# Kernel optimization log

Measured on AMD Instinct MI355X. Metric: run time of the kernel, lower is better.

Reference implementation:

```python
import jax, jax.numpy as jnp
import numpy as np

N = 10000      # nodes
ND = 64        # node_dim
H = 128        # hidden_dim
L = 4          # num_layers
K = 16         # knn k
TD = 16        # time_dim


def _time_embed(t, n):
    # sinusoidal embedding, matches _time_embed: freqs = exp(linspace(0,1,half)*-4)
    half = TD // 2
    freqs = jnp.exp(jnp.linspace(0.0, 1.0, half) * -4.0)            # [half]
    angles = t.reshape(1, 1) * freqs[None, :]                        # [1, half]
    emb = jnp.concatenate([jnp.sin(angles), jnp.cos(angles)], -1)    # [1, TD]
    return jnp.broadcast_to(emb, (n, TD))


def _knn_edges(pos, k):
    # full cdist + topk, mirroring _knn_graph (no_grad in torch)
    n = pos.shape[0]
    sq = jnp.sum(pos * pos, -1)
    d2 = sq[:, None] + sq[None, :] - 2.0 * (pos @ pos.T)             # [N, N]
    idxr = jnp.arange(n)
    d2 = d2.at[idxr, idxr].set(jnp.inf)
    _, nbr = jax.lax.top_k(-d2, k)                                   # [N, K] nearest
    src = jnp.repeat(idxr, k)
    dst = nbr.reshape(-1)
    return src, dst


def _egnn_layer(h, pos, src, dst, s, ew1, eb1, ew2, eb2, nw1, nb1, nw2, nb2, cw, cb):
    n = h.shape[0]
    diff = pos[dst] - pos[src]                                       # [E, 3]
    r2 = jnp.sum(diff * diff, -1, keepdims=True)                     # [E, 1]
    r = jnp.sqrt(r2 + 1e-8)
    dir_ij = diff / r
    e_in = jnp.concatenate([h[dst], h[src], r2], -1)                 # [E, 2H+1]
    m = jax.nn.silu(e_in @ ew1 + eb1)
    m = jax.nn.silu(m @ ew2 + eb2)                                   # [E, H]
    m = m * s[src][:, None]                                          # s-gate
    m_sum = jax.ops.segment_sum(m, dst, num_segments=n)              # [N, H]
    deg = jax.ops.segment_sum(jnp.ones((m.shape[0], 1), m.dtype), dst, num_segments=n)
    deg = jnp.maximum(deg, 1.0)
    m_sum = m_sum / deg
    hn = jax.nn.silu(jnp.concatenate([h, m_sum], -1) @ nw1 + nb1)
    h_new = hn @ nw2 + nb2                                           # [N, H]
    gamma = m @ cw + cb                                              # [E, 1]
    cu = jax.ops.segment_sum(gamma * dir_ij, dst, num_segments=n) / deg
    return h_new, pos + cu


def setup_inputs() -> dict:
    key = jax.random.key(0)
    ks = jax.random.split(key, 24)
    g = lambda k, shape: (jax.random.normal(k, shape, dtype=jnp.float32) * 0.05)
    z = lambda shape: jnp.zeros(shape, jnp.float32)
    return {
        'x': jax.random.normal(ks[0], (N, ND), jnp.float32),
        'pos': jax.random.normal(ks[1], (N, 3), jnp.float32) * 5.0,
        't': jax.random.uniform(ks[2], (1,), jnp.float32),
        's': jax.random.uniform(ks[3], (N,), jnp.float32),
        'proj_w': g(ks[4], (ND + 1 + TD, H)), 'proj_b': z((H,)),
        'edge_w1': g(ks[5], (L, 2 * H + 1, H)), 'edge_b1': z((L, H)),
        'edge_w2': g(ks[6], (L, H, H)), 'edge_b2': z((L, H)),
        'node_w1': g(ks[7], (L, 2 * H, H)), 'node_b1': z((L, H)),
        'node_w2': g(ks[8], (L, H, H)), 'node_b2': z((L, H)),
        'coord_w': g(ks[9], (L, H, 1)), 'coord_b': z((L, 1)),
        'ec_w': g(ks[10], (H, 3)), 'ec_b': z((3,)),
        'ef_w': g(ks[11], (H, ND)), 'ef_b': z((ND,)),
    }


def reference(x, pos, t, s, proj_w, proj_b, edge_w1, edge_b1, edge_w2, edge_b2,
              node_w1, node_b1, node_w2, node_b2, coord_w, coord_b,
              ec_w, ec_b, ef_w, ef_b):
    n = x.shape[0]
    src, dst = _knn_edges(jax.lax.stop_gradient(pos), K)  # graph build is no_grad
    temb = _time_embed(t[0], n)
    h = jnp.concatenate([x, s[:, None], temb], -1) @ proj_w + proj_b  # [N, H]
    p = pos
    for l in range(L):
        h, p = _egnn_layer(h, p, src, dst, s,
                           edge_w1[l], edge_b1[l], edge_w2[l], edge_b2[l],
                           node_w1[l], node_b1[l], node_w2[l], node_b2[l],
                           coord_w[l], coord_b[l])
    eps_c = h @ ec_w + ec_b                                           # [N, 3]
    eps_f = h @ ef_w + ef_b                                           # [N, ND]
    return jnp.concatenate([eps_c, eps_f, p], -1)                     # [N, 3+ND+3]
```

## Files before the change

kernel.cpp:

```cpp
#include <hip/hip_runtime.h>
#include <math.h>

#define N_NODES 10000
#define ND 64
#define H 128
#define LAYERS 4
#define KNN 16
#define TD 16
#define E_EDGES (N_NODES * KNN)
#define KC 1250
#define TILE_E 128

typedef __attribute__((ext_vector_type(8))) short short8;
typedef __attribute__((ext_vector_type(4))) float f32x4;

__device__ __forceinline__ float silu(float x) {
  return x * __builtin_amdgcn_rcpf(1.0f + __expf(-x));
}

__device__ __forceinline__ unsigned short f2bf(float f) {
  unsigned int u = __float_as_uint(f);
  u += 0x7fffu + ((u >> 16) & 1u);
  return (unsigned short)(u >> 16);
}
__device__ __forceinline__ float bf2f(unsigned short h) {
  return __uint_as_float(((unsigned int)h) << 16);
}

__global__ __launch_bounds__(256) void pos4_kernel(const float* __restrict__ pos,
                                                   float4* __restrict__ pos4,
                                                   float* __restrict__ p0,
                                                   int* __restrict__ degi) {
  int i = blockIdx.x * 256 + threadIdx.x;
  if (i >= N_NODES) return;
  float x = pos[i * 3 + 0], y = pos[i * 3 + 1], z = pos[i * 3 + 2];
  pos4[i] = make_float4(x, y, z, x * x + y * y + z * z);
  p0[i * 3 + 0] = x;
  p0[i * 3 + 1] = y;
  p0[i * 3 + 2] = z;
  degi[i] = 0;
}

__global__ __launch_bounds__(256) void wcvt_kernel(
    const float* __restrict__ ew2, const float* __restrict__ nw1,
    const float* __restrict__ nw2, const float* __restrict__ ew1,
    const float* __restrict__ pw, const float* __restrict__ ecw,
    const float* __restrict__ efw, unsigned short* __restrict__ w2T,
    unsigned short* __restrict__ nw1T, unsigned short* __restrict__ nw2T,
    unsigned short* __restrict__ ew1T, unsigned short* __restrict__ pwT,
    unsigned short* __restrict__ owT) {
  int i = blockIdx.x * 256 + threadIdx.x;
  if (i < 65536) {
    int l = i >> 14, rem = i & 16383, c = rem >> 7, o = rem & 127;
    w2T[l * 16384 + o * 128 + c] = f2bf(ew2[i]);
  } else if (i < 196608) {
    int j = i - 65536;
    int l = j >> 15, rem = j & 32767, c2 = rem >> 7, o = rem & 127;
    nw1T[l * 32768 + o * 256 + c2] = f2bf(nw1[j]);
  } else if (i < 262144) {
    int j = i - 196608;
    int l = j >> 14, rem = j & 16383, c = rem >> 7, o = rem & 127;
    nw2T[l * 16384 + o * 128 + c] = f2bf(nw2[j]);
  } else if (i < 393216) {
    int j = i - 262144;
    int l = j >> 15, rem = j & 32767, r = rem >> 7, o = rem & 127;
    int o2 = o + ((r >> 7) << 7);
    int c = r & 127;
    ew1T[l * 32768 + o2 * 128 + c] = f2bf(ew1[l * 257 * 128 + r * 128 + o]);
  } else if (i < 405504) {
    int j = i - 393216;
    int o = j / 96, c = j - o * 96;
    pwT[j] = (c < 81) ? f2bf(pw[c * 128 + o]) : 0;
  } else {
    int j = i - 405504;
    int o = j >> 7, c = j & 127;
    float v = 0.0f;
    if (o < 3) v = ecw[c * 3 + o];
    else if (o < 67) v = efw[c * 64 + (o - 3)];
    owT[j] = f2bf(v);
  }
}

#define INS(dval, gbase, V, ID, TH)                                   \
  {                                                                   \
    unsigned long long mask = __ballot((dval) < (TH));                \
    while (mask) {                                                    \
      int sl = __ffsll((long long)mask) - 1;                          \
      mask &= mask - 1;                                               \
      float db = __shfl((dval), sl, 64);                              \
      if (db >= (TH)) continue;                                       \
      int gj = (gbase) + sl;                                          \
      float pv = __shfl_up((V), 1, 64);                               \
      int pid = __shfl_up((ID), 1, 64);                               \
      bool stay = ((V) <= db);                                        \
      bool tk = (lane == 0) || (pv <= db);                            \
      (V) = stay ? (V) : (tk ? db : pv);                              \
      (ID) = stay ? (ID) : (tk ? gj : pid);                           \
      (TH) = __shfl((V), 16, 64);                                     \
    }                                                                 \
  }

__global__ __launch_bounds__(256) void knn_kernel(const float4* __restrict__ pos4,
                                                  int* __restrict__ nbr,
                                                  int* __restrict__ degi) {
  __shared__ float4 C[KC];
  int tid = threadIdx.x;
  int lane = tid & 63;
  int wid = tid >> 6;
  int qb = blockIdx.x * 8 + wid * 2;
  float4 q0 = pos4[qb];
  float4 q1 = pos4[qb + 1];
  float v0 = __builtin_inff(), v1 = __builtin_inff();
  int id0 = 0, id1 = 0;
  float th0 = __builtin_inff(), th1 = __builtin_inff();
  for (int base = 0; base < N_NODES; base += KC) {
    int cnt = min(KC, N_NODES - base);
    __syncthreads();
    for (int jj = tid; jj < cnt; jj += 256) C[jj] = pos4[base + jj];
    __syncthreads();
    for (int j0 = 0; j0 < cnt; j0 += 256) {
      float dA0 = __builtin_inff(), dA1 = __builtin_inff();
      float dB0 = __builtin_inff(), dB1 = __builtin_inff();
      float dC0 = __builtin_inff(), dC1 = __builtin_inff();
      float dD0 = __builtin_inff(), dD1 = __builtin_inff();
      int ja = j0 + lane, jbx = j0 + 64 + lane;
      int jc = j0 + 128 + lane, jd = j0 + 192 + lane;
      if (ja < cnt) {
        float4 p = C[ja];
        dA0 = fmaf(-2.0f, fmaf(q0.x, p.x, fmaf(q0.y, p.y, q0.z * p.z)), p.w);
        dA1 = fmaf(-2.0f, fmaf(q1.x, p.x, fmaf(q1.y, p.y, q1.z * p.z)), p.w);
      }
      if (jbx < cnt) {
        float4 p = C[jbx];
        dB0 = fmaf(-2.0f, fmaf(q0.x, p.x, fmaf(q0.y, p.y, q0.z * p.z)), p.w);
        dB1 = fmaf(-2.0f, fmaf(q1.x, p.x, fmaf(q1.y, p.y, q1.z * p.z)), p.w);
      }
      if (jc < cnt) {
        float4 p = C[jc];
        dC0 = fmaf(-2.0f, fmaf(q0.x, p.x, fmaf(q0.y, p.y, q0.z * p.z)), p.w);
        dC1 = fmaf(-2.0f, fmaf(q1.x, p.x, fmaf(q1.y, p.y, q1.z * p.z)), p.w);
      }
      if (jd < cnt) {
        float4 p = C[jd];
        dD0 = fmaf(-2.0f, fmaf(q0.x, p.x, fmaf(q0.y, p.y, q0.z * p.z)), p.w);
        dD1 = fmaf(-2.0f, fmaf(q1.x, p.x, fmaf(q1.y, p.y, q1.z * p.z)), p.w);
      }
      int gb = base + j0;
      float m0 = fminf(fminf(dA0, dB0), fminf(dC0, dD0));
      if (__ballot(m0 < th0)) {
        INS(dA0, gb, v0, id0, th0);
        INS(dB0, gb + 64, v0, id0, th0);
        INS(dC0, gb + 128, v0, id0, th0);
        INS(dD0, gb + 192, v0, id0, th0);
      }
      float m1 = fminf(fminf(dA1, dB1), fminf(dC1, dD1));
      if (__ballot(m1 < th1)) {
        INS(dA1, gb, v1, id1, th1);
        INS(dB1, gb + 64, v1, id1, th1);
        INS(dC1, gb + 128, v1, id1, th1);
        INS(dD1, gb + 192, v1, id1, th1);
      }
    }
  }
  if (lane >= 1 && lane < 17) {
    nbr[qb * KNN + lane - 1] = id0;
    atomicAdd(&degi[id0], 1);
    nbr[(qb + 1) * KNN + lane - 1] = id1;
    atomicAdd(&degi[id1], 1);
  }
}

__global__ __launch_bounds__(1024) void scan_kernel(const int* __restrict__ degi,
                                                    int* __restrict__ off,
                                                    int* __restrict__ cursor) {
  __shared__ int part[1024];
  int t = threadIdx.x;
  int base = t * 10;
  int sum = 0;
  if (t < 1000)
    for (int i = 0; i < 10; ++i) sum += degi[base + i];
  part[t] = sum;
  __syncthreads();
  for (int stp = 1; stp < 1024; stp <<= 1) {
    int v = (t >= stp) ? part[t - stp] : 0;
    __syncthreads();
    part[t] += v;
    __syncthreads();
  }
  if (t < 1000) {
    int run = (t == 0) ? 0 : part[t - 1];
    for (int i = 0; i < 10; ++i) {
      off[base + i] = run;
      cursor[base + i] = run;
      run += degi[base + i];
    }
  }
  if (t == 0) off[N_NODES] = E_EDGES;
}

__global__ void scatter_kernel(const int* __restrict__ nbr, int* __restrict__ cursor,
                               int* __restrict__ eid, int* __restrict__ dstof) {
  int e = blockIdx.x * 256 + threadIdx.x;
  if (e < E_EDGES) {
    int d = nbr[e];
    int p = atomicAdd(&cursor[d], 1);
    eid[p] = e;
    dstof[p] = d;
  }
}

__global__ void sort_kernel(const int* __restrict__ off, int* __restrict__ eid) {
  int n = blockIdx.x * 256 + threadIdx.x;
  if (n >= N_NODES) return;
  int a = off[n], b = off[n + 1];
  for (int i = a + 1; i < b; ++i) {
    int v = eid[i];
    int j = i - 1;
    while (j >= a && eid[j] > v) { eid[j + 1] = eid[j]; --j; }
    eid[j + 1] = v;
  }
}

__global__ __launch_bounds__(256) void proj_ab_kernel(
    const float* __restrict__ x, const float* __restrict__ s,
    const float* __restrict__ tptr, const unsigned short* __restrict__ pwT,
    const float* __restrict__ pb, const unsigned short* __restrict__ ew1T,
    const float* __restrict__ eb1, float* __restrict__ h_out,
    unsigned short* __restrict__ Abf, unsigned short* __restrict__ Bbf) {
  __shared__ unsigned short inpb[16][104];
  __shared__ unsigned short hb[16][136];
  int tid = threadIdx.x;
  int n0 = blockIdx.x * 16;
  float t = tptr[0];
  for (int idx = tid; idx < 16 * 104; idx += 256) {
    int n = idx / 104, c = idx - n * 104;
    int gn = n0 + n;
    float val;
    if (c < 64) val = x[gn * ND + c];
    else if (c == 64) val = s[gn];
    else if (c < 81) {
      int j = c - 65;
      int jj = (j < 8) ? j : (j - 8);
      float f = __expf(-4.0f * (float)jj / 7.0f);
      float a = t * f;
      val = (j < 8) ? sinf(a) : cosf(a);
    } else val = 0.0f;
    inpb[n][c] = f2bf(val);
  }
  __syncthreads();
  int w = tid >> 6, lane = tid & 63, fr = lane & 15, kg = lane >> 4;
  f32x4 acc[2];
  acc[0] = (f32x4){0.f, 0.f, 0.f, 0.f};
  acc[1] = (f32x4){0.f, 0.f, 0.f, 0.f};
#pragma unroll
  for (int ks = 0; ks < 3; ++ks) {
    int k = ks * 32 + kg * 8;
    short8 a = *(const short8*)&inpb[fr][k];
#pragma unroll
    for (int nt = 0; nt < 2; ++nt) {
      int col = w * 32 + nt * 16 + fr;
      short8 b = *(const short8*)&pwT[col * 96 + k];
      acc[nt] = __builtin_amdgcn_mfma_f32_16x16x32_bf16(a, b, acc[nt], 0, 0, 0);
    }
  }
#pragma unroll
  for (int nt = 0; nt < 2; ++nt) {
    int col = w * 32 + nt * 16 + fr;
    float bias = pb[col];
#pragma unroll
    for (int r = 0; r < 4; ++r) {
      int row = kg * 4 + r;
      float hv = acc[nt][r] + bias;
      h_out[(n0 + row) * H + col] = hv;
      hb[row][col] = f2bf(hv);
    }
  }
  __syncthreads();
  f32x4 acc2[4];
#pragma unroll
  for (int nt = 0; nt < 4; ++nt) acc2[nt] = (f32x4){0.f, 0.f, 0.f, 0.f};
#pragma unroll
  for (int ks = 0; ks < 4; ++ks) {
    int k = ks * 32 + kg * 8;
    short8 a = *(const short8*)&hb[fr][k];
#pragma unroll
    for (int nt = 0; nt < 4; ++nt) {
      int col = w * 64 + nt * 16 + fr;
      short8 b = *(const short8*)&ew1T[col * H + k];
      acc2[nt] = __builtin_amdgcn_mfma_f32_16x16x32_bf16(a, b, acc2[nt], 0, 0, 0);
    }
  }
#pragma unroll
  for (int nt = 0; nt < 4; ++nt) {
    int col = w * 64 + nt * 16 + fr;
    float bias = (col < H) ? eb1[col] : 0.0f;
#pragma unroll
    for (int r = 0; r < 4; ++r) {
      int row = kg * 4 + r;
      float val = acc2[nt][r] + bias;
      if (col < H) Abf[(n0 + row) * H + col] = f2bf(val);
      else Bbf[(n0 + row) * H + (col - H)] = f2bf(val);
    }
  }
}

__global__ __launch_bounds__(256) void edge_mfma_kernel(
    const unsigned short* __restrict__ Abf, const unsigned short* __restrict__ Bbf,
    const float* __restrict__ p, const float* __restrict__ s,
    const int* __restrict__ csr_off, const int* __restrict__ eid,
    const int* __restrict__ dstof, const float* __restrict__ wr,
    const unsigned short* __restrict__ w2T, const float* __restrict__ eb2,
    const float* __restrict__ cw, const float* __restrict__ cbp,
    float* __restrict__ msA, float* __restrict__ msB,
    float* __restrict__ cuA, float* __restrict__ cuB) {
  __shared__ unsigned short t1s[TILE_E][136];
  __shared__ float r2A[TILE_E], sA[TILE_E], dirA[TILE_E][3], gA[TILE_E];
  __shared__ float gpart[2][TILE_E];
  __shared__ int srcA[TILE_E], dstA[TILE_E];
  __shared__ float wrs[H], b2s[H], cws[H];

  int tid = threadIdx.x;
  int P0 = blockIdx.x * TILE_E;
  int P1 = P0 + TILE_E;

  if (tid < H) { wrs[tid] = wr[tid]; b2s[tid] = eb2[tid]; cws[tid] = cw[tid]; }
  if (tid < TILE_E) {
    int e = tid;
    int edge = eid[P0 + e];
    int src = edge >> 4;
    int d = dstof[P0 + e];
    srcA[e] = src;
    dstA[e] = d;
    float dx = p[d * 3 + 0] - p[src * 3 + 0];
    float dy = p[d * 3 + 1] - p[src * 3 + 1];
    float dz = p[d * 3 + 2] - p[src * 3 + 2];
    float r2 = dx * dx + dy * dy + dz * dz;
    r2A[e] = r2;
    float rinv = 1.0f / sqrtf(r2 + 1e-8f);
    dirA[e][0] = dx * rinv;
    dirA[e][1] = dy * rinv;
    dirA[e][2] = dz * rinv;
    sA[e] = s[src];
  }
  __syncthreads();

  int nA = dstA[0], nB = dstA[TILE_E - 1];
  int nn = nB - nA + 1;

  for (int idx = tid; idx < TILE_E * 32; idx += 256) {
    int e = idx >> 5, cp = (idx & 31) * 4;
    uint2 au = *(const uint2*)&Abf[dstA[e] * H + cp];
    uint2 bu = *(const uint2*)&Bbf[srcA[e] * H + cp];
    float r2v = r2A[e];
    float pr0 = silu(bf2f((unsigned short)(au.x & 0xffffu)) +
                     bf2f((unsigned short)(bu.x & 0xffffu)) + r2v * wrs[cp]);
    float pr1 = silu(bf2f((unsigned short)(au.x >> 16)) +
                     bf2f((unsigned short)(bu.x >> 16)) + r2v * wrs[cp + 1]);
    float pr2 = silu(bf2f((unsigned short)(au.y & 0xffffu)) +
                     bf2f((unsigned short)(bu.y & 0xffffu)) + r2v * wrs[cp + 2]);
    float pr3 = silu(bf2f((unsigned short)(au.y >> 16)) +
                     bf2f((unsigned short)(bu.y >> 16)) + r2v * wrs[cp + 3]);
    uint2 o;
    o.x = ((unsigned int)f2bf(pr1) << 16) | (unsigned int)f2bf(pr0);
    o.y = ((unsigned int)f2bf(pr3) << 16) | (unsigned int)f2bf(pr2);
    *(uint2*)&t1s[e][cp] = o;
  }
  __syncthreads();

  int w = tid >> 6, lane = tid & 63;
  int fr = lane & 15, kg = lane >> 4;
  f32x4 acc[8][2];
#pragma unroll
  for (int mt = 0; mt < 8; ++mt)
#pragma unroll
    for (int nt = 0; nt < 2; ++nt) acc[mt][nt] = (f32x4){0.f, 0.f, 0.f, 0.f};
#pragma unroll
  for (int ks = 0; ks < 4; ++ks) {
    int k = ks * 32 + kg * 8;
    short8 bf0 = *(const short8*)&w2T[(w * 32 + fr) * H + k];
    short8 bf1 = *(const short8*)&w2T[(w * 32 + 16 + fr) * H + k];
#pragma unroll
    for (int mt = 0; mt < 8; ++mt) {
      short8 a = *(const short8*)&t1s[mt * 16 + fr][k];
      acc[mt][0] = __builtin_amdgcn_mfma_f32_16x16x32_bf16(a, bf0, acc[mt][0], 0, 0, 0);
      acc[mt][1] = __builtin_amdgcn_mfma_f32_16x16x32_bf16(a, bf1, acc[mt][1], 0, 0, 0);
    }
  }
  __syncthreads();

#pragma unroll
  for (int mt = 0; mt < 8; ++mt) {
#pragma unroll
    for (int nt = 0; nt < 2; ++nt) {
      int col = w * 32 + nt * 16 + fr;
      float b2v = b2s[col];
#pragma unroll
      for (int r = 0; r < 4; ++r) {
        int row = mt * 16 + kg * 4 + r;
        float mv = silu(acc[mt][nt][r] + b2v) * sA[row];
        t1s[row][col] = f2bf(mv);
      }
    }
  }
  __syncthreads();

  {
    int e = tid & 127, half = tid >> 7;
    int c0 = half * 64;
    float g = 0.f;
    for (int c = c0; c < c0 + 64; c += 4) {
      uint2 u = *(const uint2*)&t1s[e][c];
      g = fmaf(bf2f((unsigned short)(u.x & 0xffffu)), cws[c], g);
      g = fmaf(bf2f((unsigned short)(u.x >> 16)), cws[c + 1], g);
      g = fmaf(bf2f((unsigned short)(u.y & 0xffffu)), cws[c + 2], g);
      g = fmaf(bf2f((unsigned short)(u.y >> 16)), cws[c + 3], g);
    }
    gpart[half][e] = g;
  }
  __syncthreads();
  if (tid < TILE_E) gA[tid] = gpart[0][tid] + gpart[1][tid] + cbp[0];
  __syncthreads();

  for (int idx = tid; idx < nn * 32; idx += 256) {
    int ni = idx >> 5, cq = (idx & 31) * 4;
    int n = nA + ni;
    int o0 = csr_off[n], o1 = csr_off[n + 1];
    int lo = max(o0, P0), hi = min(o1, P1);
    float s0 = 0.f, s1 = 0.f, s2 = 0.f, s3 = 0.f;
    for (int pos = lo; pos < hi; ++pos) {
      uint2 u = *(const uint2*)&t1s[pos - P0][cq];
      s0 += bf2f((unsigned short)(u.x & 0xffffu));
      s1 += bf2f((unsigned short)(u.x >> 16));
      s2 += bf2f((unsigned short)(u.y & 0xffffu));
      s3 += bf2f((unsigned short)(u.y >> 16));
    }
    float4 sv = make_float4(s0, s1, s2, s3);
    if (o0 >= P0) {
      *(float4*)&msA[n * H + cq] = sv;
      if (o1 <= P1) *(float4*)&msB[n * H + cq] = make_float4(0.f, 0.f, 0.f, 0.f);
    } else {
      *(float4*)&msB[n * H + cq] = sv;
    }
  }
  for (int idx = tid; idx < nn * 3; idx += 256) {
    int ni = idx / 3, comp = idx - ni * 3;
    int n = nA + ni;
    int o0 = csr_off[n], o1 = csr_off[n + 1];
    int lo = max(o0, P0), hi = min(o1, P1);
    float sum = 0.f;
    for (int pos = lo; pos < hi; ++pos)
      sum += gA[pos - P0] * dirA[pos - P0][comp];
    if (o0 >= P0) {
      cuA[n * 3 + comp] = sum;
      if (o1 <= P1) cuB[n * 3 + comp] = 0.0f;
    } else {
      cuB[n * 3 + comp] = sum;
    }
  }
}

__global__ __launch_bounds__(256) void node_mfma_kernel(
    const float* __restrict__ h, const float* __restrict__ msA,
    const float* __restrict__ msB, const int* __restrict__ degi,
    const float* __restrict__ cuA, const float* __restrict__ cuB,
    const float* __restrict__ p_in, const unsigned short* __restrict__ w1T,
    const float* __restrict__ nb1, const unsigned short* __restrict__ w2T,
    const float* __restrict__ nb2, const unsigned short* __restrict__ ew1Tn,
    const float* __restrict__ eb1n, int doab, float* __restrict__ h_out,
    float* __restrict__ p_out, unsigned short* __restrict__ Abf,
    unsigned short* __restrict__ Bbf) {
  __shared__ unsigned short insb[16][264];
  __shared__ unsigned short hnsb[16][136];
  int tid = threadIdx.x;
  int n0 = blockIdx.x * 16;
  for (int idx = tid; idx < 16 * H; idx += 256) {
    int n = idx >> 7, c = idx & 127;
    int gn = n0 + n;
    float hv = h[gn * H + c];
    int dg = degi[gn];
    float ms = 0.f;
    if (dg > 0) ms = (msA[gn * H + c] + msB[gn * H + c]) / (float)dg;
    insb[n][c] = f2bf(hv);
    insb[n][H + c] = f2bf(ms);
  }
  __syncthreads();
  int w = tid >> 6, lane = tid & 63, fr = lane & 15, kg = lane >> 4;
  f32x4 acc[2];
  acc[0] = (f32x4){0.f, 0.f, 0.f, 0.f};
  acc[1] = (f32x4){0.f, 0.f, 0.f, 0.f};
#pragma unroll
  for (int ks = 0; ks < 8; ++ks) {
    int k = ks * 32 + kg * 8;
    short8 a = *(const short8*)&insb[fr][k];
#pragma unroll
    for (int nt = 0; nt < 2; ++nt) {
      int col = w * 32 + nt * 16 + fr;
      short8 b = *(const short8*)&w1T[col * 256 + k];
      acc[nt] = __builtin_amdgcn_mfma_f32_16x16x32_bf16(a, b, acc[nt], 0, 0, 0);
    }
  }
#pragma unroll
  for (int nt = 0; nt < 2; ++nt) {
    int col = w * 32 + nt * 16 + fr;
    float b1 = nb1[col];
#pragma unroll
    for (int r = 0; r < 4; ++r) {
      int row = kg * 4 + r;
      hnsb[row][col] = f2bf(silu(acc[nt][r] + b1));
    }
  }
  __syncthreads();
  f32x4 acc2[2];
  acc2[0] = (f32x4){0.f, 0.f, 0.f, 0.f};
  acc2[1] = (f32x4){0.f, 0.f, 0.f, 0.f};
#pragma unroll
  for (int ks = 0; ks < 4; ++ks) {
    int k = ks * 32 + kg * 8;
    short8 a = *(const short8*)&hnsb[fr][k];
#pragma unroll
    for (int nt = 0; nt < 2; ++nt) {
      int col = w * 32 + nt * 16 + fr;
      short8 b = *(const short8*)&w2T[col * H + k];
      acc2[nt] = __builtin_amdgcn_mfma_f32_16x16x32_bf16(a, b, acc2[nt], 0, 0, 0);
    }
  }
  unsigned short (*hb)[136] = (unsigned short(*)[136])insb;
#pragma unroll
  for (int nt = 0; nt < 2; ++nt) {
    int col = w * 32 + nt * 16 + fr;
    float b2 = nb2[col];
#pragma unroll
    for (int r = 0; r < 4; ++r) {
      int row = kg * 4 + r;
      float hv = acc2[nt][r] + b2;
      h_out[(n0 + row) * H + col] = hv;
      hb[row][col] = f2bf(hv);
    }
  }
  if (tid < 48) {
    int nl = tid / 3, comp = tid - nl * 3;
    int gn = n0 + nl;
    int dg = degi[gn];
    float add = 0.0f;
    if (dg > 0)
      add = (cuA[gn * 3 + comp] + cuB[gn * 3 + comp]) / (float)dg;
    p_out[gn * 3 + comp] = p_in[gn * 3 + comp] + add;
  }
  if (doab) {
    __syncthreads();
    f32x4 acc3[4];
#pragma unroll
    for (int nt = 0; nt < 4; ++nt) acc3[nt] = (f32x4){0.f, 0.f, 0.f, 0.f};
#pragma unroll
    for (int ks = 0; ks < 4; ++ks) {
      int k = ks * 32 + kg * 8;
      short8 a = *(const short8*)&hb[fr][k];
#pragma unroll
      for (int nt = 0; nt < 4; ++nt) {
        int col = w * 64 + nt * 16 + fr;
        short8 b = *(const short8*)&ew1Tn[col * H + k];
        acc3[nt] = __builtin_amdgcn_mfma_f32_16x16x32_bf16(a, b, acc3[nt], 0, 0, 0);
      }
    }
#pragma unroll
    for (int nt = 0; nt < 4; ++nt) {
      int col = w * 64 + nt * 16 + fr;
      float bias = (col < H) ? eb1n[col] : 0.0f;
#pragma unroll
      for (int r = 0; r < 4; ++r) {
        int row = kg * 4 + r;
        float val = acc3[nt][r] + bias;
        if (col < H) Abf[(n0 + row) * H + col] = f2bf(val);
        else Bbf[(n0 + row) * H + (col - H)] = f2bf(val);
      }
    }
  }
}

__global__ __launch_bounds__(256) void out_mfma_kernel(
    const float* __restrict__ h, const float* __restrict__ p,
    const unsigned short* __restrict__ owT, const float* __restrict__ ecb,
    const float* __restrict__ efb, float* __restrict__ out) {
  __shared__ unsigned short hb[16][136];
  int tid = threadIdx.x;
  int n0 = blockIdx.x * 16;
  for (int idx = tid; idx < 16 * H; idx += 256) {
    int n = idx >> 7, c = idx & 127;
    hb[n][c] = f2bf(h[(n0 + n) * H + c]);
  }
  __syncthreads();
  int w = tid >> 6, lane = tid & 63, fr = lane & 15, kg = lane >> 4;
  int ntiles = (w == 0) ? 2 : 1;
  for (int tt = 0; tt < ntiles; ++tt) {
    int tile = (tt == 0) ? w : 4;
    f32x4 acc = (f32x4){0.f, 0.f, 0.f, 0.f};
    int col = tile * 16 + fr;
#pragma unroll
    for (int ks = 0; ks < 4; ++ks) {
      int k = ks * 32 + kg * 8;
      short8 a = *(const short8*)&hb[fr][k];
      short8 b = *(const short8*)&owT[col * H + k];
      acc = __builtin_amdgcn_mfma_f32_16x16x32_bf16(a, b, acc, 0, 0, 0);
    }
    if (col < 67) {
      float bias = (col < 3) ? ecb[col] : efb[col - 3];
#pragma unroll
      for (int r = 0; r < 4; ++r) {
        int row = kg * 4 + r;
        out[(n0 + row) * 70 + col] = acc[r] + bias;
      }
    }
  }
  if (tid < 48) {
    int nl = tid / 3, comp = tid - nl * 3;
    int gn = n0 + nl;
    out[gn * 70 + 67 + comp] = p[gn * 3 + comp];
  }
}

extern "C" void kernel_launch(void* const* d_in, const int* in_sizes, int n_in,
                              void* d_out, int out_size, void* d_ws, size_t ws_size,
                              hipStream_t stream) {
  const float* x = (const float*)d_in[0];
  const float* pos = (const float*)d_in[1];
  const float* t = (const float*)d_in[2];
  const float* s = (const float*)d_in[3];
  const float* pw = (const float*)d_in[4];
  const float* pb = (const float*)d_in[5];
  const float* ew1 = (const float*)d_in[6];
  const float* eb1 = (const float*)d_in[7];
  const float* ew2 = (const float*)d_in[8];
  const float* eb2 = (const float*)d_in[9];
  const float* nw1 = (const float*)d_in[10];
  const float* nb1 = (const float*)d_in[11];
  const float* nw2 = (const float*)d_in[12];
  const float* nb2 = (const float*)d_in[13];
  const float* cw = (const float*)d_in[14];
  const float* cb = (const float*)d_in[15];
  const float* ecw = (const float*)d_in[16];
  const float* ecb = (const float*)d_in[17];
  const float* efw = (const float*)d_in[18];
  const float* efb = (const float*)d_in[19];

  char* wp = (char*)d_ws;
  auto alloc = [&](size_t bytes) {
    char* r = wp;
    wp += (bytes + 255) & ~(size_t)255;
    return r;
  };
  float* h0 = (float*)alloc((size_t)N_NODES * H * 4);
  float* h1 = (float*)alloc((size_t)N_NODES * H * 4);
  unsigned short* Abf = (unsigned short*)alloc((size_t)N_NODES * H * 2);
  unsigned short* Bbf = (unsigned short*)alloc((size_t)N_NODES * H * 2);
  float* msAb = (float*)alloc((size_t)N_NODES * H * 4);
  float* msBb = (float*)alloc((size_t)N_NODES * H * 4);
  float* cuAb = (float*)alloc((size_t)N_NODES * 3 * 4);
  float* cuBb = (float*)alloc((size_t)N_NODES * 3 * 4);
  float* p0 = (float*)alloc((size_t)N_NODES * 3 * 4);
  float* p1 = (float*)alloc((size_t)N_NODES * 3 * 4);
  int* degi = (int*)alloc((size_t)N_NODES * 4);
  int* nbr = (int*)alloc((size_t)E_EDGES * 4);
  int* off = (int*)alloc((size_t)(N_NODES + 1) * 4);
  int* cursor = (int*)alloc((size_t)N_NODES * 4);
  int* eid = (int*)alloc((size_t)E_EDGES * 4);
  int* dstof = (int*)alloc((size_t)E_EDGES * 4);
  unsigned short* w2Tb = (unsigned short*)alloc((size_t)LAYERS * H * H * 2);
  unsigned short* nw1Tb = (unsigned short*)alloc((size_t)LAYERS * 2 * H * H * 2);
  unsigned short* nw2Tb = (unsigned short*)alloc((size_t)LAYERS * H * H * 2);
  unsigned short* ew1Tb = (unsigned short*)alloc((size_t)LAYERS * 2 * H * H * 2);
  unsigned short* pwTb = (unsigned short*)alloc((size_t)H * 96 * 2);
  unsigned short* owTb = (unsigned short*)alloc((size_t)80 * H * 2);

  float4* pos4 = (float4*)msAb;

  wcvt_kernel<<<1624, 256, 0, stream>>>(ew2, nw1, nw2, ew1, pw, ecw, efw,
                                        w2Tb, nw1Tb, nw2Tb, ew1Tb, pwTb, owTb);
  pos4_kernel<<<(N_NODES + 255) / 256, 256, 0, stream>>>(pos, pos4, p0, degi);
  knn_kernel<<<N_NODES / 8, 256, 0, stream>>>(pos4, nbr, degi);
  scan_kernel<<<1, 1024, 0, stream>>>(degi, off, cursor);
  scatter_kernel<<<(E_EDGES + 255) / 256, 256, 0, stream>>>(nbr, cursor, eid, dstof);
  sort_kernel<<<(N_NODES + 255) / 256, 256, 0, stream>>>(off, eid);
  proj_ab_kernel<<<N_NODES / 16, 256, 0, stream>>>(x, s, t, pwTb, pb, ew1Tb, eb1,
                                                   h0, Abf, Bbf);

  float* hc = h0;
  float* hn = h1;
  float* pc = p0;
  float* pn = p1;
  for (int l = 0; l < LAYERS; ++l) {
    const float* ew1l = ew1 + (size_t)l * 257 * H;
    int doab = (l < LAYERS - 1) ? 1 : 0;
    edge_mfma_kernel<<<E_EDGES / TILE_E, 256, 0, stream>>>(
        Abf, Bbf, pc, s, off, eid, dstof, ew1l + 256 * H,
        w2Tb + (size_t)l * H * H, eb2 + l * H, cw + l * H, cb + l,
        msAb, msBb, cuAb, cuBb);
    node_mfma_kernel<<<N_NODES / 16, 256, 0, stream>>>(
        hc, msAb, msBb, degi, cuAb, cuBb, pc, nw1Tb + (size_t)l * 2 * H * H,
        nb1 + l * H, nw2Tb + (size_t)l * H * H, nb2 + l * H,
        ew1Tb + (size_t)(l + doab) * 2 * H * H, eb1 + (size_t)(l + doab) * H,
        doab, hn, pn, Abf, Bbf);
    float* tmp = hc; hc = hn; hn = tmp;
    tmp = pc; pc = pn; pn = tmp;
  }
  out_mfma_kernel<<<N_NODES / 16, 256, 0, stream>>>(hc, pc, owTb, ecb, efb,
                                                    (float*)d_out);
}
```

Measured before the change: 428.9 us.

## Specialize KNN scan loop, interleave dual-query insertion, widen edge and node loads

The KNN kernel drops per-element bounds checks by hardcoding the 1250-candidate chunk (four full 256-wide steps plus a tail block), folds the -2 scale into the query coefficients, and interleaves the insertion loops for both queries behind a single ballot. The edge kernel's first-layer staging now loads 16-byte bf16 vectors instead of 8-byte ones. The node kernel's input staging uses float4 loads and packed bf16 stores. Together these target instruction overhead and memory transaction count. The hardcoded tail relies on N being a multiple of KC with the remainder fixed at 1250.

```diff
diff --git a/kernel.cpp b/kernel.cpp
--- a/kernel.cpp
+++ b/kernel.cpp
@@ -81,23 +81,46 @@
   }
 }
 
-#define INS(dval, gbase, V, ID, TH)                                   \
-  {                                                                   \
-    unsigned long long mask = __ballot((dval) < (TH));                \
-    while (mask) {                                                    \
-      int sl = __ffsll((long long)mask) - 1;                          \
-      mask &= mask - 1;                                               \
-      float db = __shfl((dval), sl, 64);                              \
-      if (db >= (TH)) continue;                                       \
-      int gj = (gbase) + sl;                                          \
-      float pv = __shfl_up((V), 1, 64);                               \
-      int pid = __shfl_up((ID), 1, 64);                               \
-      bool stay = ((V) <= db);                                        \
-      bool tk = (lane == 0) || (pv <= db);                            \
-      (V) = stay ? (V) : (tk ? db : pv);                              \
-      (ID) = stay ? (ID) : (tk ? gj : pid);                           \
-      (TH) = __shfl((V), 16, 64);                                     \
-    }                                                                 \
+#define DIST2(pp, d0, d1)                                                    \
+  d0 = fmaf(ax0, (pp).x, fmaf(ay0, (pp).y, fmaf(az0, (pp).z, (pp).w)));      \
+  d1 = fmaf(ax1, (pp).x, fmaf(ay1, (pp).y, fmaf(az1, (pp).z, (pp).w)));
+
+#define PAIR(dv0, dv1, gbase)                                                \
+  {                                                                          \
+    unsigned long long m0 = __ballot((dv0) < th0);                           \
+    unsigned long long m1 = __ballot((dv1) < th1);                           \
+    while (m0 | m1) {                                                        \
+      if (m0) {                                                              \
+        int sl = __ffsll((long long)m0) - 1;                                 \
+        m0 &= m0 - 1;                                                        \
+        float db = __shfl((dv0), sl, 64);                                    \
+        if (db < th0) {                                                      \
+          int gj = (gbase) + sl;                                             \
+          float pv = __shfl_up(v0, 1, 64);                                   \
+          int pid = __shfl_up(id0, 1, 64);                                   \
+          bool stay = (v0 <= db);                                            \
+          bool tk = (lane == 0) || (pv <= db);                               \
+          v0 = stay ? v0 : (tk ? db : pv);                                   \
+          id0 = stay ? id0 : (tk ? gj : pid);                                \
+          th0 = __shfl(v0, 16, 64);                                          \
+        }                                                                    \
+      }                                                                      \
+      if (m1) {                                                              \
+        int sl = __ffsll((long long)m1) - 1;                                 \
+        m1 &= m1 - 1;                                                        \
+        float db = __shfl((dv1), sl, 64);                                    \
+        if (db < th1) {                                                      \
+          int gj = (gbase) + sl;                                             \
+          float pv = __shfl_up(v1, 1, 64);                                   \
+          int pid = __shfl_up(id1, 1, 64);                                   \
+          bool stay = (v1 <= db);                                            \
+          bool tk = (lane == 0) || (pv <= db);                               \
+          v1 = stay ? v1 : (tk ? db : pv);                                   \
+          id1 = stay ? id1 : (tk ? gj : pid);                                \
+          th1 = __shfl(v1, 16, 64);                                          \
+        }                                                                    \
+      }                                                                      \
+    }                                                                        \
   }
 
 __global__ __launch_bounds__(256) void knn_kernel(const float4* __restrict__ pos4,
@@ -110,55 +133,52 @@
   int qb = blockIdx.x * 8 + wid * 2;
   float4 q0 = pos4[qb];
   float4 q1 = pos4[qb + 1];
+  float ax0 = -2.0f * q0.x, ay0 = -2.0f * q0.y, az0 = -2.0f * q0.z;
+  float ax1 = -2.0f * q1.x, ay1 = -2.0f * q1.y, az1 = -2.0f * q1.z;
   float v0 = __builtin_inff(), v1 = __builtin_inff();
   int id0 = 0, id1 = 0;
   float th0 = __builtin_inff(), th1 = __builtin_inff();
   for (int base = 0; base < N_NODES; base += KC) {
-    int cnt = min(KC, N_NODES - base);
     __syncthreads();
-    for (int jj = tid; jj < cnt; jj += 256) C[jj] = pos4[base + jj];
+    for (int jj = tid; jj < KC; jj += 256) C[jj] = pos4[base + jj];
     __syncthreads();
-    for (int j0 = 0; j0 < cnt; j0 += 256) {
-      float dA0 = __builtin_inff(), dA1 = __builtin_inff();
-      float dB0 = __builtin_inff(), dB1 = __builtin_inff();
-      float dC0 = __builtin_inff(), dC1 = __builtin_inff();
+    for (int j0 = 0; j0 < 1024; j0 += 256) {
+      float4 pA = C[j0 + lane], pB = C[j0 + 64 + lane];
+      float4 pC = C[j0 + 128 + lane], pD = C[j0 + 192 + lane];
+      float dA0, dA1, dB0, dB1, dC0, dC1, dD0, dD1;
+      DIST2(pA, dA0, dA1);
+      DIST2(pB, dB0, dB1);
+      DIST2(pC, dC0, dC1);
+      DIST2(pD, dD0, dD1);
+      float mn0 = fminf(fminf(dA0, dB0), fminf(dC0, dD0));
+      float mn1 = fminf(fminf(dA1, dB1), fminf(dC1, dD1));
+      if (__ballot((mn0 < th0) | (mn1 < th1))) {
+        int gb = base + j0;
+        PAIR(dA0, dA1, gb);
+        PAIR(dB0, dB1, gb + 64);
+        PAIR(dC0, dC1, gb + 128);
+        PAIR(dD0, dD1, gb + 192);
+      }
+    }
+    {
+      float4 pA = C[1024 + lane], pB = C[1088 + lane], pC = C[1152 + lane];
+      float dA0, dA1, dB0, dB1, dC0, dC1;
       float dD0 = __builtin_inff(), dD1 = __builtin_inff();
-      int ja = j0 + lane, jbx = j0 + 64 + lane;
-      int jc = j0 + 128 + lane, jd = j0 + 192 + lane;
-      if (ja < cnt) {
-        float4 p = C[ja];
-        dA0 = fmaf(-2.0f, fmaf(q0.x, p.x, fmaf(q0.y, p.y, q0.z * p.z)), p.w);
-        dA1 = fmaf(-2.0f, fmaf(q1.x, p.x, fmaf(q1.y, p.y, q1.z * p.z)), p.w);
+      DIST2(pA, dA0, dA1);
+      DIST2(pB, dB0, dB1);
+      DIST2(pC, dC0, dC1);
+      if (lane < 34) {
+        float4 pD = C[1216 + lane];
+        DIST2(pD, dD0, dD1);
       }
-      if (jbx < cnt) {
-        float4 p = C[jbx];
-        dB0 = fmaf(-2.0f, fmaf(q0.x, p.x, fmaf(q0.y, p.y, q0.z * p.z)), p.w);
-        dB1 = fmaf(-2.0f, fmaf(q1.x, p.x, fmaf(q1.y, p.y, q1.z * p.z)), p.w);
-      }
-      if (jc < cnt) {
-        float4 p = C[jc];
-        dC0 = fmaf(-2.0f, fmaf(q0.x, p.x, fmaf(q0.y, p.y, q0.z * p.z)), p.w);
-        dC1 = fmaf(-2.0f, fmaf(q1.x, p.x, fmaf(q1.y, p.y, q1.z * p.z)), p.w);
-      }
-      if (jd < cnt) {
-        float4 p = C[jd];
-        dD0 = fmaf(-2.0f, fmaf(q0.x, p.x, fmaf(q0.y, p.y, q0.z * p.z)), p.w);
-        dD1 = fmaf(-2.0f, fmaf(q1.x, p.x, fmaf(q1.y, p.y, q1.z * p.z)), p.w);
-      }
-      int gb = base + j0;
-      float m0 = fminf(fminf(dA0, dB0), fminf(dC0, dD0));
-      if (__ballot(m0 < th0)) {
-        INS(dA0, gb, v0, id0, th0);
-        INS(dB0, gb + 64, v0, id0, th0);
-        INS(dC0, gb + 128, v0, id0, th0);
-        INS(dD0, gb + 192, v0, id0, th0);
-      }
-      float m1 = fminf(fminf(dA1, dB1), fminf(dC1, dD1));
-      if (__ballot(m1 < th1)) {
-        INS(dA1, gb, v1, id1, th1);
-        INS(dB1, gb + 64, v1, id1, th1);
-        INS(dC1, gb + 128, v1, id1, th1);
-        INS(dD1, gb + 192, v1, id1, th1);
+      float mn0 = fminf(fminf(dA0, dB0), fminf(dC0, dD0));
+      float mn1 = fminf(fminf(dA1, dB1), fminf(dC1, dD1));
+      if (__ballot((mn0 < th0) | (mn1 < th1))) {
+        int gb = base + 1024;
+        PAIR(dA0, dA1, gb);
+        PAIR(dB0, dB1, gb + 64);
+        PAIR(dC0, dC1, gb + 128);
+        PAIR(dD0, dD1, gb + 192);
       }
     }
   }
@@ -347,23 +367,25 @@
   int nA = dstA[0], nB = dstA[TILE_E - 1];
   int nn = nB - nA + 1;
 
-  for (int idx = tid; idx < TILE_E * 32; idx += 256) {
-    int e = idx >> 5, cp = (idx & 31) * 4;
-    uint2 au = *(const uint2*)&Abf[dstA[e] * H + cp];
-    uint2 bu = *(const uint2*)&Bbf[srcA[e] * H + cp];
+  for (int idx = tid; idx < TILE_E * 16; idx += 256) {
+    int e = idx >> 4, cp = (idx & 15) * 8;
+    uint4 au = *(const uint4*)&Abf[dstA[e] * H + cp];
+    uint4 bu = *(const uint4*)&Bbf[srcA[e] * H + cp];
     float r2v = r2A[e];
-    float pr0 = silu(bf2f((unsigned short)(au.x & 0xffffu)) +
-                     bf2f((unsigned short)(bu.x & 0xffffu)) + r2v * wrs[cp]);
-    float pr1 = silu(bf2f((unsigned short)(au.x >> 16)) +
-                     bf2f((unsigned short)(bu.x >> 16)) + r2v * wrs[cp + 1]);
-    float pr2 = silu(bf2f((unsigned short)(au.y & 0xffffu)) +
-                     bf2f((unsigned short)(bu.y & 0xffffu)) + r2v * wrs[cp + 2]);
-    float pr3 = silu(bf2f((unsigned short)(au.y >> 16)) +
-                     bf2f((unsigned short)(bu.y >> 16)) + r2v * wrs[cp + 3]);
-    uint2 o;
-    o.x = ((unsigned int)f2bf(pr1) << 16) | (unsigned int)f2bf(pr0);
-    o.y = ((unsigned int)f2bf(pr3) << 16) | (unsigned int)f2bf(pr2);
-    *(uint2*)&t1s[e][cp] = o;
+    unsigned int as[4] = {au.x, au.y, au.z, au.w};
+    unsigned int bs[4] = {bu.x, bu.y, bu.z, bu.w};
+    unsigned int res[4];
+#pragma unroll
+    for (int q = 0; q < 4; ++q) {
+      float pr0 = silu(bf2f((unsigned short)(as[q] & 0xffffu)) +
+                       bf2f((unsigned short)(bs[q] & 0xffffu)) +
+                       r2v * wrs[cp + 2 * q]);
+      float pr1 = silu(bf2f((unsigned short)(as[q] >> 16)) +
+                       bf2f((unsigned short)(bs[q] >> 16)) +
+                       r2v * wrs[cp + 2 * q + 1]);
+      res[q] = ((unsigned int)f2bf(pr1) << 16) | (unsigned int)f2bf(pr0);
+    }
+    *(uint4*)&t1s[e][cp] = make_uint4(res[0], res[1], res[2], res[3]);
   }
   __syncthreads();
 
@@ -473,15 +495,28 @@
   __shared__ unsigned short hnsb[16][136];
   int tid = threadIdx.x;
   int n0 = blockIdx.x * 16;
-  for (int idx = tid; idx < 16 * H; idx += 256) {
-    int n = idx >> 7, c = idx & 127;
+  for (int idx = tid; idx < 16 * 32; idx += 256) {
+    int n = idx >> 5, cq = (idx & 31) * 4;
     int gn = n0 + n;
-    float hv = h[gn * H + c];
+    float4 hv = *(const float4*)&h[gn * H + cq];
     int dg = degi[gn];
-    float ms = 0.f;
-    if (dg > 0) ms = (msA[gn * H + c] + msB[gn * H + c]) / (float)dg;
-    insb[n][c] = f2bf(hv);
-    insb[n][H + c] = f2bf(ms);
+    float m0 = 0.f, m1 = 0.f, m2 = 0.f, m3 = 0.f;
+    if (dg > 0) {
+      float4 a = *(const float4*)&msA[gn * H + cq];
+      float4 b = *(const float4*)&msB[gn * H + cq];
+      float fdg = (float)dg;
+      m0 = (a.x + b.x) / fdg;
+      m1 = (a.y + b.y) / fdg;
+      m2 = (a.z + b.z) / fdg;
+      m3 = (a.w + b.w) / fdg;
+    }
+    uint2 uh, um;
+    uh.x = ((unsigned int)f2bf(hv.y) << 16) | (unsigned int)f2bf(hv.x);
+    uh.y = ((unsigned int)f2bf(hv.w) << 16) | (unsigned int)f2bf(hv.z);
+    um.x = ((unsigned int)f2bf(m1) << 16) | (unsigned int)f2bf(m0);
+    um.y = ((unsigned int)f2bf(m3) << 16) | (unsigned int)f2bf(m2);
+    *(uint2*)&insb[n][cq] = uh;
+    *(uint2*)&insb[n][H + cq] = um;
   }
   __syncthreads();
   int w = tid >> 6, lane = tid & 63, fr = lane & 15, kg = lane >> 4;
```

Result: faster. 401.2 us (-6.5%).
